# Kernel tuning notes

Hardware: AMD Instinct MI355X
Metric: run time of the kernel (lower is better)

## Reference

```python
import jax, jax.numpy as jnp
import numpy as np

B, T, N, H = 4, 256, 16, 256
NHEAD = 8
FFN = 1024
WIN = 8
EPS = 1e-5


def setup_inputs() -> dict:
    key = jax.random.key(0)
    ks = jax.random.split(key, 10)
    s = 0.02
    return {
        "x": jax.random.normal(ks[0], (B, T, N, H), dtype=jnp.float32),
        "key_padding_mask": jnp.zeros((B, T, N), dtype=bool),
        "Wq": jax.random.normal(ks[1], (H, H), dtype=jnp.float32) * s,
        "bq": jnp.zeros((H,), dtype=jnp.float32),
        "Wk": jax.random.normal(ks[2], (H, H), dtype=jnp.float32) * s,
        "bk": jnp.zeros((H,), dtype=jnp.float32),
        "Wv": jax.random.normal(ks[3], (H, H), dtype=jnp.float32) * s,
        "bv": jnp.zeros((H,), dtype=jnp.float32),
        "W1": jax.random.normal(ks[4], (H, FFN), dtype=jnp.float32) * s,
        "b1": jnp.zeros((FFN,), dtype=jnp.float32),
        "W2": jax.random.normal(ks[5], (FFN, H), dtype=jnp.float32) * s,
        "b2": jnp.zeros((H,), dtype=jnp.float32),
        "g1": jnp.ones((H,), dtype=jnp.float32),
        "beta1": jnp.zeros((H,), dtype=jnp.float32),
        "g2": jnp.ones((H,), dtype=jnp.float32),
        "beta2": jnp.zeros((H,), dtype=jnp.float32),
    }


def _layer_norm(x, g, b):
    m = jnp.mean(x, axis=-1, keepdims=True)
    v = jnp.mean(jnp.square(x - m), axis=-1, keepdims=True)
    return (x - m) * jax.lax.rsqrt(v + EPS) * g + b


def reference(x, key_padding_mask, Wq, bq, Wk, bk, Wv, bv, W1, b1, W2, b2, g1, beta1, g2, beta2):
    Bq, Tq, Nq, Hq = x.shape
    D = Hq // NHEAD
    W = 2 * WIN + 1
    # projections
    q = (x @ Wq + bq).reshape(Bq, Tq, Nq, NHEAD, D) / np.float32(np.sqrt(D))
    k = (x @ Wk + bk).reshape(Bq, Tq, Nq, NHEAD, D)
    v = (x @ Wv + bv).reshape(Bq, Tq, Nq, NHEAD, D)
    idx = jnp.arange(Tq)[:, None] + jnp.arange(W)[None, :] - WIN  # (T, W)
    valid = (idx >= 0) & (idx < Tq)                               # (T, W)
    cidx = jnp.clip(idx, 0, Tq - 1)
    vf6 = valid.reshape(1, Tq, W, 1, 1, 1).astype(q.dtype)
    # gathered window keys/values, zero outside clip: (B, T, W, N, h, D)
    wk = jnp.take(k, cidx, axis=1) * vf6
    wv = jnp.take(v, cidx, axis=1) * vf6
    # attention logits over (W, N) neighbors per head
    logits = jnp.einsum('btnhd,btwmhd->btnwmh', q, wk)  # (B,T,N,W,N,h)
    # mask: padded detections within window, plus out-of-range frames
    kpm_g = jnp.take(key_padding_mask, cidx, axis=1)          # (B,T,W,N)
    mask = jnp.where(valid[None, :, :, None], kpm_g, True)    # (B,T,W,N)
    logits = jnp.where(mask[:, :, None, :, :, None], -jnp.inf, logits)
    attn = jax.nn.softmax(logits.reshape(Bq, Tq, Nq, W * Nq, NHEAD), axis=-2)
    ctx = jnp.einsum('btnmh,btmhd->btnhd', attn,
                     wv.reshape(Bq, Tq, W * Nq, NHEAD, D)).reshape(Bq, Tq, Nq, Hq)
    # residual + LN + FFN + residual + LN (dropout = identity in eval)
    y = _layer_norm(x + ctx, g1, beta1)
    ff = jax.nn.relu(y @ W1 + b1) @ W2 + b2
    return _layer_norm(y + ff, g2, beta2)
```

## Files before the change

kernel.cpp:

```cpp
#include <hip/hip_runtime.h>
#include <hip/hip_bf16.h>
#include <math.h>

typedef __attribute__((ext_vector_type(8))) short short8;
typedef __attribute__((ext_vector_type(4))) float float4v;

#define BB 4
#define TT 256
#define NDET 16
#define HH 256
#define NHEAD 8
#define DD 32
#define FFNDIM 1024
#define ROWS (BB*TT*NDET)
#define EPS 1e-5f

__device__ __forceinline__ unsigned short f2bf(float f) {
  unsigned int u = __float_as_uint(f);
  u += 0x7fffu + ((u >> 16) & 1u);
  return (unsigned short)(u >> 16);
}
__device__ __forceinline__ float bf2f(unsigned short u) {
  return __uint_as_float((unsigned int)u << 16);
}
__device__ __forceinline__ float exp2v(float x) {
  float r; asm("v_exp_f32 %0, %1" : "=v"(r) : "v"(x)); return r;
}
__device__ __forceinline__ unsigned int cvtpk(float lo, float hi) {
  unsigned int r; asm("v_cvt_pk_bf16_f32 %0, %1, %2" : "=v"(r) : "v"(lo), "v"(hi)); return r;
}

__device__ __forceinline__ void wt_tile(const float* __restrict__ W, unsigned short* __restrict__ WT,
                                        int K, int N, int k0, int n0,
                                        float (*tile)[33], int tid) {
  {
    int r = tid >> 3, c4 = (tid & 7) * 4;
    float4 in = *(const float4*)(W + (size_t)(k0 + r) * N + n0 + c4);
    tile[r][c4 + 0] = in.x; tile[r][c4 + 1] = in.y;
    tile[r][c4 + 2] = in.z; tile[r][c4 + 3] = in.w;
  }
  __syncthreads();
  {
    int n = tid >> 3, k4 = (tid & 7) * 4;
    ushort4 o;
    o.x = f2bf(tile[k4 + 0][n]); o.y = f2bf(tile[k4 + 1][n]);
    o.z = f2bf(tile[k4 + 2][n]); o.w = f2bf(tile[k4 + 3][n]);
    *(ushort4*)(WT + (size_t)(n0 + n) * K + k0 + k4) = o;
  }
}

__global__ void prep_kernel(const float* __restrict__ x, const unsigned char* __restrict__ kpm,
                            const float* __restrict__ Wq, const float* __restrict__ Wk,
                            const float* __restrict__ Wv, const float* __restrict__ W1,
                            const float* __restrict__ W2,
                            const float* __restrict__ bq, const float* __restrict__ bk,
                            const float* __restrict__ bv,
                            unsigned short* __restrict__ xb, unsigned short* __restrict__ WqkvT,
                            unsigned short* __restrict__ W1T, unsigned short* __restrict__ W2T,
                            unsigned short* __restrict__ kpm16, float* __restrict__ bqkv) {
  __shared__ float tile[32][33];
  int bid = blockIdx.x, tid = threadIdx.x;
  if (bid < 4096) {
    size_t i = (size_t)(bid * 256 + tid) * 4;
    float4 v = *(const float4*)(x + i);
    ushort4 o = { f2bf(v.x), f2bf(v.y), f2bf(v.z), f2bf(v.w) };
    *(ushort4*)(xb + i) = o;
  } else if (bid < 4288) {
    int t = bid - 4096;
    int wsel = t >> 6, tt = t & 63;
    const float* W = (wsel == 0) ? Wq : (wsel == 1) ? Wk : Wv;
    wt_tile(W, WqkvT + wsel * 65536, 256, 256, (tt >> 3) * 32, (tt & 7) * 32, tile, tid);
  } else if (bid < 4544) {
    int tt = bid - 4288;
    wt_tile(W1, W1T, 256, 1024, (tt >> 5) * 32, (tt & 31) * 32, tile, tid);
  } else if (bid < 4800) {
    int tt = bid - 4544;
    wt_tile(W2, W2T, 1024, 256, (tt >> 3) * 32, (tt & 7) * 32, tile, tid);
  } else if (bid < 4804) {
    int w = (bid - 4800) * 256 + tid;
    uint4 u = *(const uint4*)(kpm + (size_t)w * 16);
    unsigned int a[4] = {u.x, u.y, u.z, u.w};
    unsigned int bits = 0;
#pragma unroll
    for (int m = 0; m < 16; ++m)
      if ((a[m >> 2] >> ((m & 3) * 8)) & 0xffu) bits |= (1u << m);
    kpm16[w] = (unsigned short)bits;
  } else {
    bqkv[tid] = bq[tid];
    bqkv[256 + tid] = bk[tid];
    bqkv[512 + tid] = bv[tid];
  }
}

template<int NROWS, int K, int NT>
__device__ __forceinline__ void stage_rows(const unsigned short* __restrict__ src, int kcol0,
                                           char* ldsbase, int tid) {
  constexpr int ISS = NROWS * 8 / NT;
  int wave = tid >> 6;
#pragma unroll
  for (int i = 0; i < ISS; ++i) {
    int flat = i * (NT * 16) + tid * 16;
    int r = flat >> 7;
    int cb = flat & 127;
    int scb = cb ^ ((r & 7) << 4);
    const unsigned short* g = src + (size_t)r * K + kcol0 + (scb >> 1);
    char* l = ldsbase + i * (NT * 16) + wave * 1024;
    __builtin_amdgcn_global_load_lds((const __attribute__((address_space(1))) void*)g,
                                     (__attribute__((address_space(3))) void*)l, 16, 0, 0);
  }
}

template<int EPI>
__launch_bounds__(256, 2)
__global__ void gemm_kernel(const unsigned short* __restrict__ A,
                            const unsigned short* __restrict__ Bt,
                            const float* __restrict__ bias,
                            unsigned short* __restrict__ q_o, unsigned short* __restrict__ k_o,
                            unsigned short* __restrict__ v_o,
                            unsigned short* __restrict__ outb) {
  constexpr int BM = 128, BN = 128, K = 256, KP = K / 64;
  __shared__ char smem[(BM + BN) * 128];
  const int tid = threadIdx.x;
  const int wave = tid >> 6, lane = tid & 63;
  const int lrow = lane & 15, g = lane >> 4;
  const int m0 = blockIdx.x * BM;
  const int n0 = blockIdx.y * BN;
  const int wr = wave >> 1, wc = wave & 1;
  char* As = smem;
  char* Bs = smem + BM * 128;
  float4v acc[4][4];
#pragma unroll
  for (int i = 0; i < 4; ++i)
#pragma unroll
    for (int j = 0; j < 4; ++j) acc[i][j] = (float4v){0.f, 0.f, 0.f, 0.f};

  const unsigned short* Abase = A + (size_t)m0 * K;
  const unsigned short* Bbase = Bt + (size_t)n0 * K;
  for (int ph = 0; ph < KP; ++ph) {
    if (ph) __syncthreads();
    stage_rows<BM, K, 256>(Abase, ph * 64, As, tid);
    stage_rows<BN, K, 256>(Bbase, ph * 64, Bs, tid);
    __syncthreads();
#pragma unroll
    for (int ks = 0; ks < 2; ++ks) {
      short8 af[4], bf[4];
#pragma unroll
      for (int i = 0; i < 4; ++i) {
        int ar = wr * 64 + i * 16 + lrow;
        af[i] = *(const short8*)(As + ar * 128 + ((ks * 64 + g * 16) ^ ((ar & 7) << 4)));
      }
#pragma unroll
      for (int j = 0; j < 4; ++j) {
        int br = wc * 64 + j * 16 + lrow;
        bf[j] = *(const short8*)(Bs + br * 128 + ((ks * 64 + g * 16) ^ ((br & 7) << 4)));
      }
#pragma unroll
      for (int i = 0; i < 4; ++i)
#pragma unroll
        for (int j = 0; j < 4; ++j)
          acc[i][j] = __builtin_amdgcn_mfma_f32_16x16x32_bf16(af[i], bf[j], acc[i][j], 0, 0, 0);
    }
  }

  if (EPI == 0) {
    const float QS = 0.17677669529663687f * 1.4426950408889634f;
#pragma unroll
    for (int i = 0; i < 4; ++i)
#pragma unroll
      for (int j = 0; j < 4; ++j) {
        int C = n0 + wc * 64 + j * 16 + lrow;
        float bv = bias[C];
        int proj = C >> 8, cc = C & 255;
        int h = cc >> 5, d = cc & 31;
        unsigned short* om = (proj == 0) ? q_o : ((proj == 1) ? k_o : v_o);
        float sc = (proj == 0) ? QS : 1.f;
#pragma unroll
        for (int r = 0; r < 4; ++r) {
          int grow = m0 + wr * 64 + i * 16 + g * 4 + r;
          int b = grow >> 12, tn = grow & 4095;
          om[(size_t)((b * 8 + h) * 4096 + tn) * 32 + d] = f2bf((acc[i][j][r] + bv) * sc);
        }
      }
  } else {
#pragma unroll
    for (int i = 0; i < 4; ++i)
#pragma unroll
      for (int j = 0; j < 4; ++j) {
        int C = n0 + wc * 64 + j * 16 + lrow;
        float bv = bias[C];
#pragma unroll
        for (int r = 0; r < 4; ++r) {
          int grow = m0 + wr * 64 + i * 16 + g * 4 + r;
          outb[(size_t)grow * FFNDIM + C] = f2bf(fmaxf(acc[i][j][r] + bv, 0.f));
        }
      }
  }
}

__global__ void vt_kernel(const unsigned short* __restrict__ v, unsigned short* __restrict__ vT) {
  __shared__ unsigned short tl[64][41];
  int bh = blockIdx.x >> 6, tb = blockIdx.x & 63;
  int tid = threadIdx.x;
  {
    int r = tid >> 2, dp = (tid & 3) * 8;
    short8 in = *(const short8*)(v + ((size_t)bh * 4096 + tb * 64 + r) * 32 + dp);
#pragma unroll
    for (int j = 0; j < 8; ++j) tl[r][dp + j] = (unsigned short)in[j];
  }
  __syncthreads();
  {
    int d = tid >> 3, rp = (tid & 7) * 8;
    short8 ov;
#pragma unroll
    for (int j = 0; j < 8; ++j) ov[j] = (short)tl[rp + j][d];
    *(short8*)(vT + ((size_t)bh * 32 + d) * 4096 + tb * 64 + rp) = ov;
  }
}

__launch_bounds__(256, 4)
__global__ void attn_kernel(const unsigned short* __restrict__ qb,
                            const unsigned short* __restrict__ kb,
                            const unsigned short* __restrict__ vT,
                            const unsigned short* __restrict__ kpm16,
                            unsigned short* __restrict__ ctxb) {
  __shared__ char Pall[4][10240];
  int tid = threadIdx.x;
  int wave = tid >> 6, l = tid & 63;
  int bt = blockIdx.x >> 1;
  int h = (blockIdx.x & 1) * 4 + wave;
  int t = bt & 255, b = bt >> 8;
  char* P = Pall[wave];
  int lrow = l & 15, g = l >> 4;
  int swz = (lrow & 7) << 4;
  size_t base = (size_t)(b * 8 + h) * 4096;
  short8 qf = *(const short8*)(qb + (base + t * 16 + lrow) * 32 + g * 8);
  const float4v z4 = {0.f, 0.f, 0.f, 0.f};
  float4v s[17];
  float mx = -INFINITY;
#pragma unroll
  for (int w = 0; w < 17; ++w) {
    int j = t + w - 8;
    if (j >= 0 && j < 256) {
      short8 kf = *(const short8*)(kb + (base + j * 16 + lrow) * 32 + g * 8);
      float4v sv = __builtin_amdgcn_mfma_f32_16x16x32_bf16(kf, qf, z4, 0, 0, 0);
      unsigned int mw = kpm16[b * 256 + j];
#pragma unroll
      for (int r = 0; r < 4; ++r)
        if ((mw >> (g * 4 + r)) & 1u) sv[r] = -INFINITY;
      s[w] = sv;
#pragma unroll
      for (int r = 0; r < 4; ++r) mx = fmaxf(mx, sv[r]);
    } else {
      s[w] = (float4v){-INFINITY, -INFINITY, -INFINITY, -INFINITY};
    }
  }
  mx = fmaxf(mx, __shfl_xor(mx, 16));
  mx = fmaxf(mx, __shfl_xor(mx, 32));
  float sum = 0.f;
#pragma unroll
  for (int w = 0; w < 17; ++w)
#pragma unroll
    for (int r = 0; r < 4; ++r) {
      float e = exp2v(s[w][r] - mx);
      s[w][r] = e; sum += e;
    }
  sum += __shfl_xor(sum, 16);
  sum += __shfl_xor(sum, 32);
  float inv = 1.f / sum;
#pragma unroll
  for (int w = 0; w < 17; ++w) {
    unsigned int u0 = cvtpk(s[w][0], s[w][1]);
    unsigned int u1 = cvtpk(s[w][2], s[w][3]);
    *(unsigned int*)(P + lrow * 640 + (((w * 16 + g * 4 + 0) * 2) ^ swz)) = u0;
    *(unsigned int*)(P + lrow * 640 + (((w * 16 + g * 4 + 2) * 2) ^ swz)) = u1;
  }
  *(unsigned int*)(P + lrow * 640 + (((272 + g * 4 + 0) * 2) ^ swz)) = 0u;
  *(unsigned int*)(P + lrow * 640 + (((272 + g * 4 + 2) * 2) ^ swz)) = 0u;
  asm volatile("s_waitcnt lgkmcnt(0)" ::: "memory");
  __builtin_amdgcn_sched_barrier(0);
  float4v o0 = z4, o1 = z4;
  int tn0 = (t - 8) * 16;
  const unsigned short* vbase = vT + ((size_t)(b * 8 + h) * 32 + lrow) * 4096;
  __builtin_amdgcn_s_setprio(1);
#pragma unroll
  for (int c = 0; c < 9; ++c) {
    short8 pf = *(const short8*)(P + lrow * 640 + ((c * 64 + g * 16) ^ swz));
    short8 v0 = *(const short8*)(vbase + tn0 + c * 32 + g * 8);
    short8 v1 = *(const short8*)(vbase + (size_t)16 * 4096 + tn0 + c * 32 + g * 8);
    o0 = __builtin_amdgcn_mfma_f32_16x16x32_bf16(pf, v0, o0, 0, 0, 0);
    o1 = __builtin_amdgcn_mfma_f32_16x16x32_bf16(pf, v1, o1, 0, 0, 0);
  }
  __builtin_amdgcn_s_setprio(0);
  size_t orow = ((size_t)(b * 256 + t)) * 16;
  int col = h * 32 + lrow;
#pragma unroll
  for (int r = 0; r < 4; ++r) {
    float invn = __shfl(inv, g * 4 + r);
    size_t rr = (orow + g * 4 + r) * 256 + col;
    ctxb[rr] = f2bf(o0[r] * invn);
    ctxb[rr + 16] = f2bf(o1[r] * invn);
  }
}

__global__ void ln1_kernel(const unsigned short* __restrict__ xb,
                           const unsigned short* __restrict__ ctxb,
                           const float* __restrict__ gw, const float* __restrict__ bw,
                           unsigned short* __restrict__ yb) {
  int row = blockIdx.x * 4 + (threadIdx.x >> 6);
  int lane = threadIdx.x & 63;
  size_t bi = (size_t)row * 256 + lane * 4;
  ushort4 xv = *(const ushort4*)(xb + bi);
  ushort4 cv = *(const ushort4*)(ctxb + bi);
  float v0 = bf2f(xv.x) + bf2f(cv.x);
  float v1 = bf2f(xv.y) + bf2f(cv.y);
  float v2 = bf2f(xv.z) + bf2f(cv.z);
  float v3 = bf2f(xv.w) + bf2f(cv.w);
  float sm = v0 + v1 + v2 + v3;
  float sq = v0 * v0 + v1 * v1 + v2 * v2 + v3 * v3;
#pragma unroll
  for (int off = 32; off; off >>= 1) {
    sm += __shfl_xor(sm, off);
    sq += __shfl_xor(sq, off);
  }
  float mean = sm * (1.f / 256.f);
  float var = sq * (1.f / 256.f) - mean * mean;
  float rs = rsqrtf(var + EPS);
  float4 gv = *(const float4*)(gw + lane * 4);
  float4 bv = *(const float4*)(bw + lane * 4);
  ushort4 o;
  o.x = f2bf((v0 - mean) * rs * gv.x + bv.x);
  o.y = f2bf((v1 - mean) * rs * gv.y + bv.y);
  o.z = f2bf((v2 - mean) * rs * gv.z + bv.z);
  o.w = f2bf((v3 - mean) * rs * gv.w + bv.w);
  *(ushort4*)(yb + bi) = o;
}

__launch_bounds__(512, 2)
__global__ void ffn2_kernel(const unsigned short* __restrict__ hid,
                            const unsigned short* __restrict__ W2T,
                            const float* __restrict__ b2,
                            const unsigned short* __restrict__ yb,
                            const float* __restrict__ gw, const float* __restrict__ bw,
                            float* __restrict__ out) {
  constexpr int BM = 64, BN = 256, K = 1024, KP = K / 64;
  __shared__ char smem[(BM + BN) * 128];
  __shared__ float stats[8][32][2];
  __shared__ float mst[64], rst[64];
  const int tid = threadIdx.x;
  const int wave = tid >> 6, lane = tid & 63;
  const int lrow = lane & 15, g = lane >> 4;
  const int m0 = blockIdx.x * BM;
  const int wr = wave >> 2, wc = wave & 3;
  char* As = smem;
  char* Bs = smem + BM * 128;
  float4v acc[2][4];
#pragma unroll
  for (int i = 0; i < 2; ++i)
#pragma unroll
    for (int j = 0; j < 4; ++j) acc[i][j] = (float4v){0.f, 0.f, 0.f, 0.f};

  const unsigned short* Abase = hid + (size_t)m0 * K;
  for (int ph = 0; ph < KP; ++ph) {
    if (ph) __syncthreads();
    stage_rows<BM, K, 512>(Abase, ph * 64, As, tid);
    stage_rows<BN, K, 512>(W2T, ph * 64, Bs, tid);
    __syncthreads();
#pragma unroll
    for (int ks = 0; ks < 2; ++ks) {
      short8 af[2], bf[4];
#pragma unroll
      for (int i = 0; i < 2; ++i) {
        int ar = wr * 32 + i * 16 + lrow;
        af[i] = *(const short8*)(As + ar * 128 + ((ks * 64 + g * 16) ^ ((ar & 7) << 4)));
      }
#pragma unroll
      for (int j = 0; j < 4; ++j) {
        int br = wc * 64 + j * 16 + lrow;
        bf[j] = *(const short8*)(Bs + br * 128 + ((ks * 64 + g * 16) ^ ((br & 7) << 4)));
      }
#pragma unroll
      for (int i = 0; i < 2; ++i)
#pragma unroll
        for (int j = 0; j < 4; ++j)
          acc[i][j] = __builtin_amdgcn_mfma_f32_16x16x32_bf16(af[i], bf[j], acc[i][j], 0, 0, 0);
    }
  }
  __syncthreads();

#pragma unroll
  for (int i = 0; i < 2; ++i)
#pragma unroll
    for (int j = 0; j < 4; ++j) {
      int col = wc * 64 + j * 16 + lrow;
      float bv = b2[col];
#pragma unroll
      for (int r = 0; r < 4; ++r) {
        int row = wr * 32 + i * 16 + g * 4 + r;
        acc[i][j][r] += bv + bf2f(yb[(size_t)(m0 + row) * 256 + col]);
      }
    }
#pragma unroll
  for (int i = 0; i < 2; ++i)
#pragma unroll
    for (int r = 0; r < 4; ++r) {
      float sm = acc[i][0][r] + acc[i][1][r] + acc[i][2][r] + acc[i][3][r];
      float sq = acc[i][0][r] * acc[i][0][r] + acc[i][1][r] * acc[i][1][r]
               + acc[i][2][r] * acc[i][2][r] + acc[i][3][r] * acc[i][3][r];
#pragma unroll
      for (int off = 1; off < 16; off <<= 1) {
        sm += __shfl_xor(sm, off);
        sq += __shfl_xor(sq, off);
      }
      if (lrow == 0) {
        stats[wave][i * 16 + g * 4 + r][0] = sm;
        stats[wave][i * 16 + g * 4 + r][1] = sq;
      }
    }
  __syncthreads();
  if (tid < 64) {
    int wrr = tid >> 5, rl = tid & 31;
    float S = 0.f, Q = 0.f;
#pragma unroll
    for (int w2 = 0; w2 < 4; ++w2) {
      S += stats[wrr * 4 + w2][rl][0];
      Q += stats[wrr * 4 + w2][rl][1];
    }
    float mean = S * (1.f / 256.f);
    float var = Q * (1.f / 256.f) - mean * mean;
    mst[tid] = mean;
    rst[tid] = rsqrtf(var + EPS);
  }
  __syncthreads();
  float gv[4], bev[4];
#pragma unroll
  for (int j = 0; j < 4; ++j) {
    int col = wc * 64 + j * 16 + lrow;
    gv[j] = gw[col]; bev[j] = bw[col];
  }
#pragma unroll
  for (int i = 0; i < 2; ++i)
#pragma unroll
    for (int r = 0; r < 4; ++r) {
      int rl = wr * 32 + i * 16 + g * 4 + r;
      float mean = mst[rl], rs = rst[rl];
#pragma unroll
      for (int j = 0; j < 4; ++j) {
        int col = wc * 64 + j * 16 + lrow;
        out[(size_t)(m0 + rl) * 256 + col] = (acc[i][j][r] - mean) * rs * gv[j] + bev[j];
      }
    }
}

extern "C" void kernel_launch(void* const* d_in, const int* in_sizes, int n_in,
                              void* d_out, int out_size, void* d_ws, size_t ws_size,
                              hipStream_t stream) {
  const float* x  = (const float*)d_in[0];
  const unsigned char* kpm = (const unsigned char*)d_in[1];
  const float* Wq = (const float*)d_in[2];
  const float* bq = (const float*)d_in[3];
  const float* Wk = (const float*)d_in[4];
  const float* bk = (const float*)d_in[5];
  const float* Wv = (const float*)d_in[6];
  const float* bv = (const float*)d_in[7];
  const float* W1 = (const float*)d_in[8];
  const float* b1 = (const float*)d_in[9];
  const float* W2 = (const float*)d_in[10];
  const float* b2 = (const float*)d_in[11];
  const float* g1 = (const float*)d_in[12];
  const float* be1= (const float*)d_in[13];
  const float* g2 = (const float*)d_in[14];
  const float* be2= (const float*)d_in[15];
  float* out = (float*)d_out;

  char* w = (char*)d_ws;
  const size_t MB = 1u << 20;
  unsigned short* xb   = (unsigned short*)(w);
  unsigned short* qhm  = (unsigned short*)(w + 8 * MB);
  unsigned short* khm  = (unsigned short*)(w + 16 * MB);
  unsigned short* vhm  = (unsigned short*)(w + 24 * MB);
  unsigned short* vTb  = (unsigned short*)(w + 32 * MB);
  unsigned short* ctxb = (unsigned short*)(w + 40 * MB);
  unsigned short* yb   = (unsigned short*)(w + 48 * MB);
  unsigned short* WqkvT = (unsigned short*)(w + 72 * MB);
  unsigned short* W1T = WqkvT + 196608;
  unsigned short* W2T = W1T + 262144;
  unsigned short* kpm16 = W2T + 262144;
  float* bqkv = (float*)(kpm16 + 1024);
  unsigned short* hid = qhm;

  prep_kernel<<<4805, 256, 0, stream>>>(x, kpm, Wq, Wk, Wv, W1, W2, bq, bk, bv,
                                        xb, WqkvT, W1T, W2T, kpm16, bqkv);
  gemm_kernel<0><<<dim3(128, 6), 256, 0, stream>>>(xb, WqkvT, bqkv, qhm, khm, vhm, nullptr);
  vt_kernel<<<2048, 256, 0, stream>>>(vhm, vTb);
  attn_kernel<<<2048, 256, 0, stream>>>(qhm, khm, vTb, kpm16, ctxb);
  ln1_kernel<<<4096, 256, 0, stream>>>(xb, ctxb, g1, be1, yb);
  gemm_kernel<1><<<dim3(128, 8), 256, 0, stream>>>(yb, W1T, b1, nullptr, nullptr, nullptr, hid);
  ffn2_kernel<<<256, 512, 0, stream>>>(hid, W2T, b2, yb, g2, be2, out);
}
```

Before: 110.3 us.

## Fuse V transpose into QKV GEMM epilogue and LayerNorm1 into attention

The QKV GEMM epilogue now writes V directly in transposed (head, d, token) layout with 4-wide stores, which removes the separate vt_kernel. The attention kernel now handles all 8 heads of a frame in one 512-thread block. It adds the residual x and computes LayerNorm1 in-block through shared-memory row statistics, so the ctx buffer and ln1_kernel are gone. This saves two launches and the ctx/v round trips through memory. In exchange the attention block gets bigger, needs two block-wide syncs, and the P stride and swizzle change.

```diff
diff --git a/kernel.cpp b/kernel.cpp
--- a/kernel.cpp
+++ b/kernel.cpp
@@ -116,7 +116,7 @@
                             const unsigned short* __restrict__ Bt,
                             const float* __restrict__ bias,
                             unsigned short* __restrict__ q_o, unsigned short* __restrict__ k_o,
-                            unsigned short* __restrict__ v_o,
+                            unsigned short* __restrict__ vT_o,
                             unsigned short* __restrict__ outb) {
   constexpr int BM = 128, BN = 128, K = 256, KP = K / 64;
   __shared__ char smem[(BM + BN) * 128];
@@ -172,13 +172,24 @@
         float bv = bias[C];
         int proj = C >> 8, cc = C & 255;
         int h = cc >> 5, d = cc & 31;
-        unsigned short* om = (proj == 0) ? q_o : ((proj == 1) ? k_o : v_o);
-        float sc = (proj == 0) ? QS : 1.f;
-#pragma unroll
-        for (int r = 0; r < 4; ++r) {
-          int grow = m0 + wr * 64 + i * 16 + g * 4 + r;
-          int b = grow >> 12, tn = grow & 4095;
-          om[(size_t)((b * 8 + h) * 4096 + tn) * 32 + d] = f2bf((acc[i][j][r] + bv) * sc);
+        if (proj == 2) {
+          int grow0 = m0 + wr * 64 + i * 16 + g * 4;
+          int b = grow0 >> 12, tn0 = grow0 & 4095;
+          ushort4 o;
+          o.x = f2bf(acc[i][j][0] + bv);
+          o.y = f2bf(acc[i][j][1] + bv);
+          o.z = f2bf(acc[i][j][2] + bv);
+          o.w = f2bf(acc[i][j][3] + bv);
+          *(ushort4*)(vT_o + ((size_t)(b * 8 + h) * 32 + d) * 4096 + tn0) = o;
+        } else {
+          unsigned short* om = (proj == 0) ? q_o : k_o;
+          float sc = (proj == 0) ? QS : 1.f;
+#pragma unroll
+          for (int r = 0; r < 4; ++r) {
+            int grow = m0 + wr * 64 + i * 16 + g * 4 + r;
+            int b = grow >> 12, tn = grow & 4095;
+            om[(size_t)((b * 8 + h) * 4096 + tn) * 32 + d] = f2bf((acc[i][j][r] + bv) * sc);
+          }
         }
       }
   } else {
@@ -197,42 +208,24 @@
   }
 }
 
-__global__ void vt_kernel(const unsigned short* __restrict__ v, unsigned short* __restrict__ vT) {
-  __shared__ unsigned short tl[64][41];
-  int bh = blockIdx.x >> 6, tb = blockIdx.x & 63;
-  int tid = threadIdx.x;
-  {
-    int r = tid >> 2, dp = (tid & 3) * 8;
-    short8 in = *(const short8*)(v + ((size_t)bh * 4096 + tb * 64 + r) * 32 + dp);
-#pragma unroll
-    for (int j = 0; j < 8; ++j) tl[r][dp + j] = (unsigned short)in[j];
-  }
-  __syncthreads();
-  {
-    int d = tid >> 3, rp = (tid & 7) * 8;
-    short8 ov;
-#pragma unroll
-    for (int j = 0; j < 8; ++j) ov[j] = (short)tl[rp + j][d];
-    *(short8*)(vT + ((size_t)bh * 32 + d) * 4096 + tb * 64 + rp) = ov;
-  }
-}
-
-__launch_bounds__(256, 4)
-__global__ void attn_kernel(const unsigned short* __restrict__ qb,
-                            const unsigned short* __restrict__ kb,
-                            const unsigned short* __restrict__ vT,
-                            const unsigned short* __restrict__ kpm16,
-                            unsigned short* __restrict__ ctxb) {
-  __shared__ char Pall[4][10240];
+__launch_bounds__(512, 4)
+__global__ void attn_ln_kernel(const unsigned short* __restrict__ qb,
+                               const unsigned short* __restrict__ kb,
+                               const unsigned short* __restrict__ vT,
+                               const unsigned short* __restrict__ kpm16,
+                               const unsigned short* __restrict__ xb,
+                               const float* __restrict__ gw, const float* __restrict__ bw,
+                               unsigned short* __restrict__ yb) {
+  __shared__ char Pall[8][9216];
+  __shared__ float stats[8][16][2];
+  __shared__ float mst[16], rst[16];
   int tid = threadIdx.x;
   int wave = tid >> 6, l = tid & 63;
-  int bt = blockIdx.x >> 1;
-  int h = (blockIdx.x & 1) * 4 + wave;
-  int t = bt & 255, b = bt >> 8;
+  int t = blockIdx.x & 255, b = blockIdx.x >> 8;
   char* P = Pall[wave];
   int lrow = l & 15, g = l >> 4;
-  int swz = (lrow & 7) << 4;
-  size_t base = (size_t)(b * 8 + h) * 4096;
+  int swz = (lrow & 3) << 4;
+  size_t base = (size_t)(b * 8 + wave) * 4096;
   short8 qf = *(const short8*)(qb + (base + t * 16 + lrow) * 32 + g * 8);
   const float4v z4 = {0.f, 0.f, 0.f, 0.f};
   float4v s[17];
@@ -271,68 +264,78 @@
   for (int w = 0; w < 17; ++w) {
     unsigned int u0 = cvtpk(s[w][0], s[w][1]);
     unsigned int u1 = cvtpk(s[w][2], s[w][3]);
-    *(unsigned int*)(P + lrow * 640 + (((w * 16 + g * 4 + 0) * 2) ^ swz)) = u0;
-    *(unsigned int*)(P + lrow * 640 + (((w * 16 + g * 4 + 2) * 2) ^ swz)) = u1;
-  }
-  *(unsigned int*)(P + lrow * 640 + (((272 + g * 4 + 0) * 2) ^ swz)) = 0u;
-  *(unsigned int*)(P + lrow * 640 + (((272 + g * 4 + 2) * 2) ^ swz)) = 0u;
+    *(unsigned int*)(P + lrow * 576 + (((w * 16 + g * 4 + 0) * 2) ^ swz)) = u0;
+    *(unsigned int*)(P + lrow * 576 + (((w * 16 + g * 4 + 2) * 2) ^ swz)) = u1;
+  }
+  *(unsigned int*)(P + lrow * 576 + (((272 + g * 4 + 0) * 2) ^ swz)) = 0u;
+  *(unsigned int*)(P + lrow * 576 + (((272 + g * 4 + 2) * 2) ^ swz)) = 0u;
+
+  size_t rowbase = (size_t)(b * 256 + t) * 16 * 256;
+  int col = wave * 32 + lrow;
+  float xv0[4], xv1[4];
+#pragma unroll
+  for (int r = 0; r < 4; ++r) {
+    xv0[r] = bf2f(xb[rowbase + (g * 4 + r) * 256 + col]);
+    xv1[r] = bf2f(xb[rowbase + (g * 4 + r) * 256 + col + 16]);
+  }
+
   asm volatile("s_waitcnt lgkmcnt(0)" ::: "memory");
   __builtin_amdgcn_sched_barrier(0);
   float4v o0 = z4, o1 = z4;
   int tn0 = (t - 8) * 16;
-  const unsigned short* vbase = vT + ((size_t)(b * 8 + h) * 32 + lrow) * 4096;
+  const unsigned short* vbase = vT + (base * 32 / 4096 + lrow) * 4096;
   __builtin_amdgcn_s_setprio(1);
 #pragma unroll
   for (int c = 0; c < 9; ++c) {
-    short8 pf = *(const short8*)(P + lrow * 640 + ((c * 64 + g * 16) ^ swz));
+    short8 pf = *(const short8*)(P + lrow * 576 + ((c * 64 + g * 16) ^ swz));
     short8 v0 = *(const short8*)(vbase + tn0 + c * 32 + g * 8);
     short8 v1 = *(const short8*)(vbase + (size_t)16 * 4096 + tn0 + c * 32 + g * 8);
     o0 = __builtin_amdgcn_mfma_f32_16x16x32_bf16(pf, v0, o0, 0, 0, 0);
     o1 = __builtin_amdgcn_mfma_f32_16x16x32_bf16(pf, v1, o1, 0, 0, 0);
   }
   __builtin_amdgcn_s_setprio(0);
-  size_t orow = ((size_t)(b * 256 + t)) * 16;
-  int col = h * 32 + lrow;
+
+  float va0[4], va1[4];
 #pragma unroll
   for (int r = 0; r < 4; ++r) {
     float invn = __shfl(inv, g * 4 + r);
-    size_t rr = (orow + g * 4 + r) * 256 + col;
-    ctxb[rr] = f2bf(o0[r] * invn);
-    ctxb[rr + 16] = f2bf(o1[r] * invn);
-  }
-}
-
-__global__ void ln1_kernel(const unsigned short* __restrict__ xb,
-                           const unsigned short* __restrict__ ctxb,
-                           const float* __restrict__ gw, const float* __restrict__ bw,
-                           unsigned short* __restrict__ yb) {
-  int row = blockIdx.x * 4 + (threadIdx.x >> 6);
-  int lane = threadIdx.x & 63;
-  size_t bi = (size_t)row * 256 + lane * 4;
-  ushort4 xv = *(const ushort4*)(xb + bi);
-  ushort4 cv = *(const ushort4*)(ctxb + bi);
-  float v0 = bf2f(xv.x) + bf2f(cv.x);
-  float v1 = bf2f(xv.y) + bf2f(cv.y);
-  float v2 = bf2f(xv.z) + bf2f(cv.z);
-  float v3 = bf2f(xv.w) + bf2f(cv.w);
-  float sm = v0 + v1 + v2 + v3;
-  float sq = v0 * v0 + v1 * v1 + v2 * v2 + v3 * v3;
-#pragma unroll
-  for (int off = 32; off; off >>= 1) {
-    sm += __shfl_xor(sm, off);
-    sq += __shfl_xor(sq, off);
-  }
-  float mean = sm * (1.f / 256.f);
-  float var = sq * (1.f / 256.f) - mean * mean;
-  float rs = rsqrtf(var + EPS);
-  float4 gv = *(const float4*)(gw + lane * 4);
-  float4 bv = *(const float4*)(bw + lane * 4);
-  ushort4 o;
-  o.x = f2bf((v0 - mean) * rs * gv.x + bv.x);
-  o.y = f2bf((v1 - mean) * rs * gv.y + bv.y);
-  o.z = f2bf((v2 - mean) * rs * gv.z + bv.z);
-  o.w = f2bf((v3 - mean) * rs * gv.w + bv.w);
-  *(ushort4*)(yb + bi) = o;
+    va0[r] = o0[r] * invn + xv0[r];
+    va1[r] = o1[r] * invn + xv1[r];
+  }
+#pragma unroll
+  for (int r = 0; r < 4; ++r) {
+    float sm = va0[r] + va1[r];
+    float sq = va0[r] * va0[r] + va1[r] * va1[r];
+#pragma unroll
+    for (int off = 1; off < 16; off <<= 1) {
+      sm += __shfl_xor(sm, off);
+      sq += __shfl_xor(sq, off);
+    }
+    if (lrow == 0) {
+      stats[wave][g * 4 + r][0] = sm;
+      stats[wave][g * 4 + r][1] = sq;
+    }
+  }
+  __syncthreads();
+  if (tid < 16) {
+    float S = 0.f, Q = 0.f;
+#pragma unroll
+    for (int w2 = 0; w2 < 8; ++w2) { S += stats[w2][tid][0]; Q += stats[w2][tid][1]; }
+    float mean = S * (1.f / 256.f);
+    float var = Q * (1.f / 256.f) - mean * mean;
+    mst[tid] = mean;
+    rst[tid] = rsqrtf(var + EPS);
+  }
+  __syncthreads();
+  float gv0 = gw[col], gv1 = gw[col + 16];
+  float bv0 = bw[col], bv1 = bw[col + 16];
+#pragma unroll
+  for (int r = 0; r < 4; ++r) {
+    int row = g * 4 + r;
+    float mean = mst[row], rs = rst[row];
+    yb[rowbase + row * 256 + col]      = f2bf((va0[r] - mean) * rs * gv0 + bv0);
+    yb[rowbase + row * 256 + col + 16] = f2bf((va1[r] - mean) * rs * gv1 + bv1);
+  }
 }
 
 __launch_bounds__(512, 2)
@@ -477,9 +480,7 @@
   unsigned short* xb   = (unsigned short*)(w);
   unsigned short* qhm  = (unsigned short*)(w + 8 * MB);
   unsigned short* khm  = (unsigned short*)(w + 16 * MB);
-  unsigned short* vhm  = (unsigned short*)(w + 24 * MB);
-  unsigned short* vTb  = (unsigned short*)(w + 32 * MB);
-  unsigned short* ctxb = (unsigned short*)(w + 40 * MB);
+  unsigned short* vTb  = (unsigned short*)(w + 24 * MB);
   unsigned short* yb   = (unsigned short*)(w + 48 * MB);
   unsigned short* WqkvT = (unsigned short*)(w + 72 * MB);
   unsigned short* W1T = WqkvT + 196608;
@@ -490,10 +491,8 @@
 
   prep_kernel<<<4805, 256, 0, stream>>>(x, kpm, Wq, Wk, Wv, W1, W2, bq, bk, bv,
                                         xb, WqkvT, W1T, W2T, kpm16, bqkv);
-  gemm_kernel<0><<<dim3(128, 6), 256, 0, stream>>>(xb, WqkvT, bqkv, qhm, khm, vhm, nullptr);
-  vt_kernel<<<2048, 256, 0, stream>>>(vhm, vTb);
-  attn_kernel<<<2048, 256, 0, stream>>>(qhm, khm, vTb, kpm16, ctxb);
-  ln1_kernel<<<4096, 256, 0, stream>>>(xb, ctxb, g1, be1, yb);
+  gemm_kernel<0><<<dim3(128, 6), 256, 0, stream>>>(xb, WqkvT, bqkv, qhm, khm, vTb, nullptr);
+  attn_ln_kernel<<<1024, 512, 0, stream>>>(qhm, khm, vTb, kpm16, xb, g1, be1, yb);
   gemm_kernel<1><<<dim3(128, 8), 256, 0, stream>>>(yb, W1T, b1, nullptr, nullptr, nullptr, hid);
   ffn2_kernel<<<256, 512, 0, stream>>>(hid, W2T, b2, yb, g2, be2, out);
 }
```

After: 106.9 us. 1.03x faster.
